# Kernel tuning notes

Measured on AMD Instinct MI355X. Metric: run time of the kernel, lower is better.

## Reference

```python
import jax, jax.numpy as jnp
import numpy as np

DIM = 16  # size_in
N = 16384  # batch of samples


def _g_single(x, W1, b1, W2, b2):
    # myLinear forward for one sample x: [dim] -> [dim*dim] (symmetrized)
    h = jnp.tanh(W1 @ x + b1)                    # [dim]
    out = (W2 @ h + b2).reshape(DIM, DIM)        # [dim, dim]
    out = out + out.T                            # symmetrize (out + out.permute(0,2,1))
    return out.reshape(DIM * DIM)


def setup_inputs() -> dict:
    key = jax.random.key(0)
    k0, k1, k2, k3, k4 = jax.random.split(key, 5)
    s1 = 1.0 / np.sqrt(DIM)   # nn.Linear default init bound for fan_in=dim
    inp = jax.random.normal(k0, (N, 2 * DIM), dtype=jnp.float32)
    W1 = jax.random.uniform(k1, (DIM, DIM), dtype=jnp.float32, minval=-s1, maxval=s1)
    b1 = jax.random.uniform(k2, (DIM,), dtype=jnp.float32, minval=-s1, maxval=s1)
    W2 = jax.random.uniform(k3, (DIM * DIM, DIM), dtype=jnp.float32, minval=-s1, maxval=s1)
    b2 = jax.random.uniform(k4, (DIM * DIM,), dtype=jnp.float32, minval=-s1, maxval=s1)
    return {"t": 0, "input_": inp, "W1": W1, "b1": b1, "W2": W2, "b2": b2}


def reference(t, input_, W1, b1, W2, b2):
    x = input_[:, :DIM]   # [N, dim]
    v = input_[:, DIM:]   # [N, dim]

    g_fn = lambda xx: _g_single(xx, W1, b1, W2, b2)

    # batch jacobian of g w.r.t. x: [N, dim*dim, dim] -> [N, dim, dim, dim]
    J = jax.vmap(jax.jacfwd(g_fn))(x).reshape(N, DIM, DIM, DIM)
    g = jax.vmap(g_fn)(x).reshape(N, DIM, DIM)   # metric, symmetric
    g_inv = jnp.linalg.inv(g)                    # batched small inverse

    # faithful to the source: 4-operand einsum product (sum over l only)
    connection = 0.5 * jnp.einsum('nkl,nijl,njil,nlij->nkij', g_inv, J, J, -J)

    vv = jnp.einsum('ni,nj->nij', v, v)          # [N, dim, dim]
    dv = -jnp.einsum('hij,hkij->hk', vv, connection)  # [N, dim]

    return jnp.hstack([v, dv])                   # [N, 2*dim]
```

## Files before the change

kernel.cpp:

```cpp
#include <hip/hip_runtime.h>

#define NPTS  16384
#define BATCH 16

#define OFF_W1   0
#define OFF_B1   320
#define OFF_VB   336
#define OFF_HB   592
#define OFF_TB   848
#define OFF_XA   1104
#define OFF_U    1360
#define P_STRIDE 4352
#define LDS_FLOATS (OFF_U + 2 * P_STRIDE)

__launch_bounds__(256, 3)
__global__ void conn_kernel(const float* __restrict__ inp,
                            const float* __restrict__ W1g,
                            const float* __restrict__ b1g,
                            const float* __restrict__ W2g,
                            const float* __restrict__ b2g,
                            float* __restrict__ out)
{
    __shared__ float SH[LDS_FLOATS];
    const int tid  = threadIdx.x;
    const int i_of = tid >> 4;
    const int j_of = tid & 15;

    const int pT = (j_of << 4) | i_of;
    float s2[16];
    {
        const float4* wa = reinterpret_cast<const float4*>(W2g + tid * 16);
        const float4* wb = reinterpret_cast<const float4*>(W2g + pT  * 16);
        #pragma unroll
        for (int q = 0; q < 4; ++q) {
            float4 A = wa[q], B = wb[q];
            s2[4*q+0] = A.x + B.x;
            s2[4*q+1] = A.y + B.y;
            s2[4*q+2] = A.z + B.z;
            s2[4*q+3] = A.w + B.w;
        }
    }
    const float breg = b2g[tid] + b2g[pT];

    SH[OFF_W1 + i_of * 20 + j_of] = W1g[tid];
    if (tid < 16) SH[OFF_B1 + tid] = b1g[tid];

    const int base = blockIdx.x * BATCH;
    if (tid < 128) {
        float4 vle = reinterpret_cast<const float4*>(inp + base * 32)[tid];
        int idx = tid * 4, pt = idx >> 5, c = idx & 31;
        float* dst = (c < 16) ? &SH[OFF_XA + pt * 16 + c]
                              : &SH[OFF_VB + pt * 16 + (c - 16)];
        dst[0] = vle.x; dst[1] = vle.y; dst[2] = vle.z; dst[3] = vle.w;
    }
    __syncthreads();

    {
        const int pt = i_of, k = j_of;
        const float4* wrow = reinterpret_cast<const float4*>(&SH[OFF_W1 + k * 20]);
        const float4* xrow = reinterpret_cast<const float4*>(&SH[OFF_XA + pt * 16]);
        float pre = SH[OFF_B1 + k];
        #pragma unroll
        for (int q = 0; q < 4; ++q) {
            float4 w = wrow[q], x = xrow[q];
            pre += w.x * x.x + w.y * x.y + w.z * x.z + w.w * x.w;
        }
        float h = tanhf(pre);
        SH[OFF_HB + pt * 16 + k] = h;
        SH[OFF_TB + pt * 16 + k] = 1.0f - h * h;
    }
    __syncthreads();

    float* const P0 = &SH[OFF_U];
    float* const P1 = &SH[OFF_U + P_STRIDE];

    #pragma unroll 1
    for (int ch = 0; ch < 8; ++ch) {
        const int ptA = 2 * ch, ptB = 2 * ch + 1;

        float cA[16], cB[16], jA[16], jB[16];
        {
            const float4* tA4 = reinterpret_cast<const float4*>(&SH[OFF_TB + ptA * 16]);
            const float4* tB4 = reinterpret_cast<const float4*>(&SH[OFF_TB + ptB * 16]);
            #pragma unroll
            for (int q = 0; q < 4; ++q) {
                float4 ta = tA4[q], tb = tB4[q];
                cA[4*q+0] = s2[4*q+0] * ta.x;  cB[4*q+0] = s2[4*q+0] * tb.x;
                cA[4*q+1] = s2[4*q+1] * ta.y;  cB[4*q+1] = s2[4*q+1] * tb.y;
                cA[4*q+2] = s2[4*q+2] * ta.z;  cB[4*q+2] = s2[4*q+2] * tb.z;
                cA[4*q+3] = s2[4*q+3] * ta.w;  cB[4*q+3] = s2[4*q+3] * tb.w;
            }
        }
        #pragma unroll
        for (int l = 0; l < 16; ++l) { jA[l] = 0.f; jB[l] = 0.f; }

        #pragma unroll
        for (int k = 0; k < 16; ++k) {
            const float4* w4 = reinterpret_cast<const float4*>(&SH[OFF_W1 + k * 20]);
            float4 w0 = w4[0], w1 = w4[1], w2 = w4[2], w3 = w4[3];
            float ca = cA[k], cb = cB[k];
            jA[0]  += ca * w0.x; jA[1]  += ca * w0.y; jA[2]  += ca * w0.z; jA[3]  += ca * w0.w;
            jA[4]  += ca * w1.x; jA[5]  += ca * w1.y; jA[6]  += ca * w1.z; jA[7]  += ca * w1.w;
            jA[8]  += ca * w2.x; jA[9]  += ca * w2.y; jA[10] += ca * w2.z; jA[11] += ca * w2.w;
            jA[12] += ca * w3.x; jA[13] += ca * w3.y; jA[14] += ca * w3.z; jA[15] += ca * w3.w;
            jB[0]  += cb * w0.x; jB[1]  += cb * w0.y; jB[2]  += cb * w0.z; jB[3]  += cb * w0.w;
            jB[4]  += cb * w1.x; jB[5]  += cb * w1.y; jB[6]  += cb * w1.z; jB[7]  += cb * w1.w;
            jB[8]  += cb * w2.x; jB[9]  += cb * w2.y; jB[10] += cb * w2.z; jB[11] += cb * w2.w;
            jB[12] += cb * w3.x; jB[13] += cb * w3.y; jB[14] += cb * w3.z; jB[15] += cb * w3.w;
        }

        {
            float pfA = SH[OFF_VB + ptA * 16 + i_of] * SH[OFF_VB + ptA * 16 + j_of];
            float pfB = SH[OFF_VB + ptB * 16 + i_of] * SH[OFF_VB + ptB * 16 + j_of];
            #pragma unroll
            for (int l = 0; l < 16; ++l) {
                P0[l * 272 + j_of * 17 + i_of] = pfA * jA[l] * jA[l];
                P1[l * 272 + j_of * 17 + i_of] = pfB * jB[l] * jB[l];
            }
        }
        __syncthreads();

        {
            float sA = 0.f, sB = 0.f;
            #pragma unroll
            for (int j = 0; j < 16; ++j) {
                sA += jA[j] * P0[i_of * 272 + j * 17 + j_of];
                sB += jB[j] * P1[i_of * 272 + j * 17 + j_of];
            }
            #pragma unroll
            for (int m = 1; m < 16; m <<= 1) {
                sA += __shfl_xor(sA, m, 16);
                sB += __shfl_xor(sB, m, 16);
            }
            if (j_of == 0) {
                SH[OFF_XA + ptA * 16 + i_of] = sA;
                SH[OFF_XA + ptB * 16 + i_of] = sB;
            }
        }
        __syncthreads();
    }

    {
        float greg[16];
        #pragma unroll
        for (int pt = 0; pt < 16; ++pt) {
            const float4* h4 = reinterpret_cast<const float4*>(&SH[OFF_HB + pt * 16]);
            float g = breg;
            #pragma unroll
            for (int q = 0; q < 4; ++q) {
                float4 h = h4[q];
                g += s2[4*q+0] * h.x + s2[4*q+1] * h.y + s2[4*q+2] * h.z + s2[4*q+3] * h.w;
            }
            greg[pt] = g;
        }
        #pragma unroll
        for (int pt = 0; pt < 16; ++pt)
            SH[OFF_U + pt * 320 + i_of * 20 + j_of] = greg[pt];
    }
    __syncthreads();

    {
        const int pt = i_of, r = j_of;
        float grow[16];
        const float4* g4 = reinterpret_cast<const float4*>(&SH[OFF_U + pt * 320 + r * 20]);
        #pragma unroll
        for (int q = 0; q < 4; ++q) {
            float4 G = g4[q];
            grow[4*q+0] = G.x; grow[4*q+1] = G.y; grow[4*q+2] = G.z; grow[4*q+3] = G.w;
        }
        float rhs = SH[OFF_XA + pt * 16 + r];

        bool done = false; int myvar = 0;
        #pragma unroll
        for (int s = 0; s < 16; ++s) {
            float cand = done ? -1.0f : fabsf(grow[s]);
            float bv = cand; int bi = r;
            #pragma unroll
            for (int m = 8; m >= 1; m >>= 1) {
                float ov = __shfl_xor(bv, m, 16);
                int   oi = __shfl_xor(bi, m, 16);
                if (ov > bv || (ov == bv && oi < bi)) { bv = ov; bi = oi; }
            }
            float pv   = __shfl(grow[s], bi, 16);
            float prhs = __shfl(rhs,     bi, 16);
            float invp = 1.0f / pv;
            bool  isP  = (r == bi);
            float f    = grow[s] * invp;
            #pragma unroll
            for (int c = 0; c < 16; ++c) {
                float pc  = __shfl(grow[c], bi, 16);
                float upd = grow[c] - f * pc;
                float piv = grow[c] * invp;
                grow[c] = isP ? piv : upd;
            }
            float updr = rhs - f * prhs;
            float pivr = rhs * invp;
            rhs = isP ? pivr : updr;
            if (isP) { done = true; myvar = s; }
        }

        const int n = base + pt;
        out[n * 32 + r]           = SH[OFF_VB + pt * 16 + r];
        out[n * 32 + 16 + myvar]  = 0.5f * rhs;
    }
}

extern "C" void kernel_launch(void* const* d_in, const int* in_sizes, int n_in,
                              void* d_out, int out_size, void* d_ws, size_t ws_size,
                              hipStream_t stream) {
    const float* inp = (const float*)d_in[1];
    const float* W1  = (const float*)d_in[2];
    const float* b1  = (const float*)d_in[3];
    const float* W2  = (const float*)d_in[4];
    const float* b2  = (const float*)d_in[5];
    float* outp = (float*)d_out;
    conn_kernel<<<dim3(NPTS / BATCH), 256, 0, stream>>>(inp, W1, b1, W2, b2, outp);
}
```

Measured before the change: 121.9 us.

## Use packed FP32 FMAs for Jacobian and FP64 for metric solve

Rewrites the Jacobian accumulation with v_pk_fma_f32/v_pk_mul_f32 packed instructions. The tanh hidden layer, metric construction, contraction sums and Gauss-Jordan solve move to double precision, presumably for accuracy. The elimination loop now skips columns at or below the pivot step, and the LDS layout is reshuffled so the result vector is stored inside the P buffers. Occupancy hint goes from 3 to 4 blocks per CU. FP64 math and 64-bit shuffles add ALU and register cost, which works against the packed-math savings.

```diff
diff --git a/kernel.cpp b/kernel.cpp
--- a/kernel.cpp
+++ b/kernel.cpp
@@ -1,4 +1,6 @@
 #include <hip/hip_runtime.h>
+
+typedef float f32x2 __attribute__((ext_vector_type(2)));
 
 #define NPTS  16384
 #define BATCH 16
@@ -6,14 +8,34 @@
 #define OFF_W1   0
 #define OFF_B1   320
 #define OFF_VB   336
-#define OFF_HB   592
-#define OFF_TB   848
-#define OFF_XA   1104
+#define OFF_TB   592
+#define OFF_HBD  848
 #define OFF_U    1360
 #define P_STRIDE 4352
 #define LDS_FLOATS (OFF_U + 2 * P_STRIDE)
 
-__launch_bounds__(256, 3)
+__device__ __forceinline__ void pkfma(f32x2& d, f32x2 a, f32x2 b) {
+    asm("v_pk_fma_f32 %0, %1, %2, %0" : "+v"(d) : "v"(a), "v"(b));
+}
+__device__ __forceinline__ f32x2 pkmul(f32x2 a, f32x2 b) {
+    f32x2 d;
+    asm("v_pk_mul_f32 %0, %1, %2" : "=v"(d) : "v"(a), "v"(b));
+    return d;
+}
+__device__ __forceinline__ double shfl_d(double x, int src) {
+    long long v = __double_as_longlong(x);
+    int lo = __shfl((int)(v & 0xffffffffLL), src, 16);
+    int hi = __shfl((int)(v >> 32), src, 16);
+    return __longlong_as_double(((long long)hi << 32) | (unsigned int)lo);
+}
+__device__ __forceinline__ double shfl_xor_d(double x, int m) {
+    long long v = __double_as_longlong(x);
+    int lo = __shfl_xor((int)(v & 0xffffffffLL), m, 16);
+    int hi = __shfl_xor((int)(v >> 32), m, 16);
+    return __longlong_as_double(((long long)hi << 32) | (unsigned int)lo);
+}
+
+__launch_bounds__(256, 4)
 __global__ void conn_kernel(const float* __restrict__ inp,
                             const float* __restrict__ W1g,
                             const float* __restrict__ b1g,
@@ -27,20 +49,17 @@
     const int j_of = tid & 15;
 
     const int pT = (j_of << 4) | i_of;
-    float s2[16];
+    f32x2 s2[8];
     {
         const float4* wa = reinterpret_cast<const float4*>(W2g + tid * 16);
         const float4* wb = reinterpret_cast<const float4*>(W2g + pT  * 16);
         #pragma unroll
         for (int q = 0; q < 4; ++q) {
             float4 A = wa[q], B = wb[q];
-            s2[4*q+0] = A.x + B.x;
-            s2[4*q+1] = A.y + B.y;
-            s2[4*q+2] = A.z + B.z;
-            s2[4*q+3] = A.w + B.w;
-        }
-    }
-    const float breg = b2g[tid] + b2g[pT];
+            s2[2*q+0] = f32x2{A.x + B.x, A.y + B.y};
+            s2[2*q+1] = f32x2{A.z + B.z, A.w + B.w};
+        }
+    }
 
     SH[OFF_W1 + i_of * 20 + j_of] = W1g[tid];
     if (tid < 16) SH[OFF_B1 + tid] = b1g[tid];
@@ -49,7 +68,7 @@
     if (tid < 128) {
         float4 vle = reinterpret_cast<const float4*>(inp + base * 32)[tid];
         int idx = tid * 4, pt = idx >> 5, c = idx & 31;
-        float* dst = (c < 16) ? &SH[OFF_XA + pt * 16 + c]
+        float* dst = (c < 16) ? &SH[OFF_U  + pt * 16 + c]
                               : &SH[OFF_VB + pt * 16 + (c - 16)];
         dst[0] = vle.x; dst[1] = vle.y; dst[2] = vle.z; dst[3] = vle.w;
     }
@@ -57,17 +76,15 @@
 
     {
         const int pt = i_of, k = j_of;
-        const float4* wrow = reinterpret_cast<const float4*>(&SH[OFF_W1 + k * 20]);
-        const float4* xrow = reinterpret_cast<const float4*>(&SH[OFF_XA + pt * 16]);
-        float pre = SH[OFF_B1 + k];
-        #pragma unroll
-        for (int q = 0; q < 4; ++q) {
-            float4 w = wrow[q], x = xrow[q];
-            pre += w.x * x.x + w.y * x.y + w.z * x.z + w.w * x.w;
-        }
-        float h = tanhf(pre);
-        SH[OFF_HB + pt * 16 + k] = h;
-        SH[OFF_TB + pt * 16 + k] = 1.0f - h * h;
+        const float* wrow = &SH[OFF_W1 + k * 20];
+        const float* xrow = &SH[OFF_U  + pt * 16];
+        double pre = (double)SH[OFF_B1 + k];
+        #pragma unroll
+        for (int l = 0; l < 16; ++l)
+            pre = fma((double)wrow[l], (double)xrow[l], pre);
+        double h = tanh(pre);
+        reinterpret_cast<double*>(&SH[OFF_HBD])[pt * 16 + k] = h;
+        SH[OFF_TB + pt * 16 + k] = (float)(1.0 - h * h);
     }
     __syncthreads();
 
@@ -78,35 +95,31 @@
     for (int ch = 0; ch < 8; ++ch) {
         const int ptA = 2 * ch, ptB = 2 * ch + 1;
 
-        float cA[16], cB[16], jA[16], jB[16];
+        f32x2 cA[8], cB[8], jA[8], jB[8];
         {
-            const float4* tA4 = reinterpret_cast<const float4*>(&SH[OFF_TB + ptA * 16]);
-            const float4* tB4 = reinterpret_cast<const float4*>(&SH[OFF_TB + ptB * 16]);
-            #pragma unroll
-            for (int q = 0; q < 4; ++q) {
-                float4 ta = tA4[q], tb = tB4[q];
-                cA[4*q+0] = s2[4*q+0] * ta.x;  cB[4*q+0] = s2[4*q+0] * tb.x;
-                cA[4*q+1] = s2[4*q+1] * ta.y;  cB[4*q+1] = s2[4*q+1] * tb.y;
-                cA[4*q+2] = s2[4*q+2] * ta.z;  cB[4*q+2] = s2[4*q+2] * tb.z;
-                cA[4*q+3] = s2[4*q+3] * ta.w;  cB[4*q+3] = s2[4*q+3] * tb.w;
-            }
-        }
-        #pragma unroll
-        for (int l = 0; l < 16; ++l) { jA[l] = 0.f; jB[l] = 0.f; }
+            const f32x2* tA2 = reinterpret_cast<const f32x2*>(&SH[OFF_TB + ptA * 16]);
+            const f32x2* tB2 = reinterpret_cast<const f32x2*>(&SH[OFF_TB + ptB * 16]);
+            #pragma unroll
+            for (int m = 0; m < 8; ++m) {
+                cA[m] = pkmul(s2[m], tA2[m]);
+                cB[m] = pkmul(s2[m], tB2[m]);
+                jA[m] = f32x2{0.f, 0.f};
+                jB[m] = f32x2{0.f, 0.f};
+            }
+        }
 
         #pragma unroll
         for (int k = 0; k < 16; ++k) {
             const float4* w4 = reinterpret_cast<const float4*>(&SH[OFF_W1 + k * 20]);
             float4 w0 = w4[0], w1 = w4[1], w2 = w4[2], w3 = w4[3];
-            float ca = cA[k], cb = cB[k];
-            jA[0]  += ca * w0.x; jA[1]  += ca * w0.y; jA[2]  += ca * w0.z; jA[3]  += ca * w0.w;
-            jA[4]  += ca * w1.x; jA[5]  += ca * w1.y; jA[6]  += ca * w1.z; jA[7]  += ca * w1.w;
-            jA[8]  += ca * w2.x; jA[9]  += ca * w2.y; jA[10] += ca * w2.z; jA[11] += ca * w2.w;
-            jA[12] += ca * w3.x; jA[13] += ca * w3.y; jA[14] += ca * w3.z; jA[15] += ca * w3.w;
-            jB[0]  += cb * w0.x; jB[1]  += cb * w0.y; jB[2]  += cb * w0.z; jB[3]  += cb * w0.w;
-            jB[4]  += cb * w1.x; jB[5]  += cb * w1.y; jB[6]  += cb * w1.z; jB[7]  += cb * w1.w;
-            jB[8]  += cb * w2.x; jB[9]  += cb * w2.y; jB[10] += cb * w2.z; jB[11] += cb * w2.w;
-            jB[12] += cb * w3.x; jB[13] += cb * w3.y; jB[14] += cb * w3.z; jB[15] += cb * w3.w;
+            f32x2 wp[8] = { {w0.x,w0.y},{w0.z,w0.w},{w1.x,w1.y},{w1.z,w1.w},
+                            {w2.x,w2.y},{w2.z,w2.w},{w3.x,w3.y},{w3.z,w3.w} };
+            float ca = cA[k >> 1][k & 1], cb = cB[k >> 1][k & 1];
+            f32x2 ca2 = {ca, ca}, cb2 = {cb, cb};
+            #pragma unroll
+            for (int m = 0; m < 8; ++m) pkfma(jA[m], wp[m], ca2);
+            #pragma unroll
+            for (int m = 0; m < 8; ++m) pkfma(jB[m], wp[m], cb2);
         }
 
         {
@@ -114,94 +127,111 @@
             float pfB = SH[OFF_VB + ptB * 16 + i_of] * SH[OFF_VB + ptB * 16 + j_of];
             #pragma unroll
             for (int l = 0; l < 16; ++l) {
-                P0[l * 272 + j_of * 17 + i_of] = pfA * jA[l] * jA[l];
-                P1[l * 272 + j_of * 17 + i_of] = pfB * jB[l] * jB[l];
+                float a = jA[l >> 1][l & 1], b = jB[l >> 1][l & 1];
+                P0[l * 272 + j_of * 17 + i_of] = pfA * a * a;
+                P1[l * 272 + j_of * 17 + i_of] = pfB * b * b;
             }
         }
         __syncthreads();
 
         {
-            float sA = 0.f, sB = 0.f;
+            double sA = 0.0, sB = 0.0;
             #pragma unroll
             for (int j = 0; j < 16; ++j) {
-                sA += jA[j] * P0[i_of * 272 + j * 17 + j_of];
-                sB += jB[j] * P1[i_of * 272 + j * 17 + j_of];
+                sA = fma((double)jA[j >> 1][j & 1],
+                         (double)P0[i_of * 272 + j * 17 + j_of], sA);
+                sB = fma((double)jB[j >> 1][j & 1],
+                         (double)P1[i_of * 272 + j * 17 + j_of], sB);
             }
             #pragma unroll
             for (int m = 1; m < 16; m <<= 1) {
-                sA += __shfl_xor(sA, m, 16);
-                sB += __shfl_xor(sB, m, 16);
+                sA += shfl_xor_d(sA, m);
+                sB += shfl_xor_d(sB, m);
             }
             if (j_of == 0) {
-                SH[OFF_XA + ptA * 16 + i_of] = sA;
-                SH[OFF_XA + ptB * 16 + i_of] = sB;
+                P0[i_of * 272 + ch * 17 + 16] = (float)sA;
+                P1[i_of * 272 + ch * 17 + 16] = (float)sB;
             }
         }
         __syncthreads();
     }
 
-    {
-        float greg[16];
+    float rhsf;
+    {
+        const int pt = i_of, r = j_of;
+        const float* Pb = (pt & 1) ? P1 : P0;
+        rhsf = Pb[r * 272 + (pt >> 1) * 17 + 16];
+    }
+    __syncthreads();
+
+    {
+        double s2d[16];
+        const float4* wa = reinterpret_cast<const float4*>(W2g + tid * 16);
+        const float4* wb = reinterpret_cast<const float4*>(W2g + pT  * 16);
+        #pragma unroll
+        for (int q = 0; q < 4; ++q) {
+            float4 A = wa[q], B = wb[q];
+            s2d[4*q+0] = (double)A.x + (double)B.x;
+            s2d[4*q+1] = (double)A.y + (double)B.y;
+            s2d[4*q+2] = (double)A.z + (double)B.z;
+            s2d[4*q+3] = (double)A.w + (double)B.w;
+        }
+        double bd = (double)b2g[tid] + (double)b2g[pT];
+
+        double* GD = reinterpret_cast<double*>(&SH[OFF_U]);
+        const double* HD = reinterpret_cast<const double*>(&SH[OFF_HBD]);
         #pragma unroll
         for (int pt = 0; pt < 16; ++pt) {
-            const float4* h4 = reinterpret_cast<const float4*>(&SH[OFF_HB + pt * 16]);
-            float g = breg;
-            #pragma unroll
-            for (int q = 0; q < 4; ++q) {
-                float4 h = h4[q];
-                g += s2[4*q+0] * h.x + s2[4*q+1] * h.y + s2[4*q+2] * h.z + s2[4*q+3] * h.w;
-            }
-            greg[pt] = g;
-        }
-        #pragma unroll
-        for (int pt = 0; pt < 16; ++pt)
-            SH[OFF_U + pt * 320 + i_of * 20 + j_of] = greg[pt];
+            const double* hrow = &HD[pt * 16];
+            double acc = bd;
+            #pragma unroll
+            for (int k = 0; k < 16; ++k) acc = fma(s2d[k], hrow[k], acc);
+            GD[pt * 272 + i_of * 17 + j_of] = acc;
+        }
     }
     __syncthreads();
 
     {
         const int pt = i_of, r = j_of;
-        float grow[16];
-        const float4* g4 = reinterpret_cast<const float4*>(&SH[OFF_U + pt * 320 + r * 20]);
-        #pragma unroll
-        for (int q = 0; q < 4; ++q) {
-            float4 G = g4[q];
-            grow[4*q+0] = G.x; grow[4*q+1] = G.y; grow[4*q+2] = G.z; grow[4*q+3] = G.w;
-        }
-        float rhs = SH[OFF_XA + pt * 16 + r];
+        const double* GD = reinterpret_cast<const double*>(&SH[OFF_U]);
+        double grow[16];
+        const double* gr = &GD[pt * 272 + r * 17];
+        #pragma unroll
+        for (int c = 0; c < 16; ++c) grow[c] = gr[c];
+        double rhs = (double)rhsf;
 
         bool done = false; int myvar = 0;
         #pragma unroll
         for (int s = 0; s < 16; ++s) {
-            float cand = done ? -1.0f : fabsf(grow[s]);
-            float bv = cand; int bi = r;
+            float bv = done ? -1.0f : (float)fabs(grow[s]);
+            int bi = r;
             #pragma unroll
             for (int m = 8; m >= 1; m >>= 1) {
                 float ov = __shfl_xor(bv, m, 16);
                 int   oi = __shfl_xor(bi, m, 16);
                 if (ov > bv || (ov == bv && oi < bi)) { bv = ov; bi = oi; }
             }
-            float pv   = __shfl(grow[s], bi, 16);
-            float prhs = __shfl(rhs,     bi, 16);
-            float invp = 1.0f / pv;
-            bool  isP  = (r == bi);
-            float f    = grow[s] * invp;
-            #pragma unroll
-            for (int c = 0; c < 16; ++c) {
-                float pc  = __shfl(grow[c], bi, 16);
-                float upd = grow[c] - f * pc;
-                float piv = grow[c] * invp;
+            double pv   = shfl_d(grow[s], bi);
+            double prhs = shfl_d(rhs,     bi);
+            double invp = 1.0 / pv;
+            bool   isP  = (r == bi);
+            double f    = grow[s] * invp;
+            #pragma unroll
+            for (int c = s + 1; c < 16; ++c) {
+                double pc  = shfl_d(grow[c], bi);
+                double upd = fma(-f, pc, grow[c]);
+                double piv = grow[c] * invp;
                 grow[c] = isP ? piv : upd;
             }
-            float updr = rhs - f * prhs;
-            float pivr = rhs * invp;
+            double updr = fma(-f, prhs, rhs);
+            double pivr = rhs * invp;
             rhs = isP ? pivr : updr;
             if (isP) { done = true; myvar = s; }
         }
 
         const int n = base + pt;
-        out[n * 32 + r]           = SH[OFF_VB + pt * 16 + r];
-        out[n * 32 + 16 + myvar]  = 0.5f * rhs;
+        out[n * 32 + r]          = SH[OFF_VB + pt * 16 + r];
+        out[n * 32 + 16 + myvar] = (float)(0.5 * rhs);
     }
 }
 
```

Result: slower. 137.3 us (+12.7%).
